# Kernel optimization log

Measured on AMD Instinct MI355X. Metric: run time of the kernel, lower is better.

The kernel has to match this reference:

```python
import jax, jax.numpy as jnp
import numpy as np

B, L, D_MODEL = 8, 2048, 512
N_QUBITS, Q_LAYERS = 10, 4
DIM = 2 ** N_QUBITS
EPS = 1e-5  # torch LayerNorm default


def _apply_1q_tok(state, U, q):
    # per-token 2x2 gate U: (N,2,2), wire 0 = most significant (PennyLane order)
    N = state.shape[0]
    s = state.reshape(N, 2 ** q, 2, -1)
    return jnp.einsum('nij,najb->naib', U, s).reshape(N, -1)


def _apply_1q(state, U, q):
    # shared 2x2 gate U: (2,2)
    N = state.shape[0]
    s = state.reshape(N, 2 ** q, 2, -1)
    return jnp.einsum('ij,najb->naib', U, s).reshape(N, -1)


def _cnot(state, c, t):
    N = state.shape[0]
    lo, hi = min(c, t), max(c, t)
    s = state.reshape(N, 2 ** lo, 2, 2 ** (hi - lo - 1), 2, -1)
    if c < t:
        # control is the first 2-axis; flip target axis where control==1
        s = s.at[:, :, 1].set(jnp.flip(s[:, :, 1], axis=3))
    else:
        # target is the first 2-axis, control the second
        s = s.at[:, :, :, :, 1].set(jnp.flip(s[:, :, :, :, 1], axis=2))
    return s.reshape(N, -1)


def _simulate(feats, weights):
    # feats: (N, n_qubits) angles; weights: (q_layers, n_qubits, 2)
    N = feats.shape[0]
    half = 0.5 * feats
    cxa = jnp.cos(half).astype(jnp.complex64)
    sxa = jnp.sin(half).astype(jnp.complex64)
    phz = jnp.exp(1j * half.astype(jnp.complex64))  # e^{+i theta/2}
    state = jnp.zeros((N, DIM), jnp.complex64).at[:, 0].set(1.0 + 0j)
    for l in range(Q_LAYERS):
        # AngleEmbedding rotation='X' : RX(feat_q) on wire q
        for q in range(N_QUBITS):
            c, s = cxa[:, q], sxa[:, q]
            U = jnp.stack([jnp.stack([c, -1j * s], -1),
                           jnp.stack([-1j * s, c], -1)], -2)  # (N,2,2)
            state = _apply_1q_tok(state, U, q)
        # AngleEmbedding rotation='Z' : RZ(feat_q) on wire q (diagonal)
        for q in range(N_QUBITS):
            p = phz[:, q]
            diag = jnp.stack([jnp.conj(p), p], -1)  # (N,2)
            s = state.reshape(N, 2 ** q, 2, -1)
            state = (s * diag[:, None, :, None]).reshape(N, -1)
        # trainable RY, RZ per wire (shared across tokens)
        for q in range(N_QUBITS):
            ty = 0.5 * weights[l, q, 0]
            cy, sy = jnp.cos(ty), jnp.sin(ty)
            Uy = jnp.stack([jnp.stack([cy, -sy]), jnp.stack([sy, cy])]).astype(jnp.complex64)
            state = _apply_1q(state, Uy, q)
            pz = jnp.exp(1j * (0.5 * weights[l, q, 1]).astype(jnp.complex64))
            diag = jnp.stack([jnp.conj(pz), pz])  # (2,)
            s = state.reshape(N, 2 ** q, 2, -1)
            state = (s * diag[None, None, :, None]).reshape(N, -1)
        # entangling CNOT ring
        for q in range(N_QUBITS):
            state = _cnot(state, q, (q + 1) % N_QUBITS)
    probs = jnp.real(state) ** 2 + jnp.imag(state) ** 2  # (N, 2**n)
    zs = []
    for q in range(N_QUBITS):
        p = probs.reshape(N, 2 ** q, 2, -1).sum(axis=(1, 3))  # (N,2)
        zs.append(p[:, 0] - p[:, 1])  # <Z_q>
    return jnp.stack(zs, -1)  # (N, n_qubits)


def setup_inputs() -> dict:
    key = jax.random.key(0)
    ks = jax.random.split(key, 4)
    x = jax.random.normal(ks[0], (B, L, D_MODEL), jnp.float32)
    in_W = jax.random.normal(ks[1], (N_QUBITS, D_MODEL), jnp.float32) / np.float32(np.sqrt(D_MODEL))
    in_b = jnp.zeros((N_QUBITS,), jnp.float32)
    gamma = jnp.ones((N_QUBITS,), jnp.float32)
    beta = jnp.zeros((N_QUBITS,), jnp.float32)
    weights = 0.05 * jax.random.normal(ks[2], (Q_LAYERS, N_QUBITS, 2), jnp.float32)
    out_W = jax.random.normal(ks[3], (D_MODEL, N_QUBITS), jnp.float32) / np.float32(np.sqrt(N_QUBITS))
    out_b = jnp.zeros((D_MODEL,), jnp.float32)
    return {"x": x, "in_W": in_W, "in_b": in_b, "gamma": gamma, "beta": beta,
            "weights": weights, "out_W": out_W, "out_b": out_b}


def reference(x, in_W, in_b, gamma, beta, weights, out_W, out_b):
    Bs, Ls, _ = x.shape
    h = jnp.tanh(jnp.einsum('bld,qd->blq', x, in_W) + in_b)
    mu = h.mean(-1, keepdims=True)
    var = ((h - mu) ** 2).mean(-1, keepdims=True)
    h = (h - mu) / jnp.sqrt(var + EPS) * gamma + beta
    q_out = _simulate(h.reshape(Bs * Ls, N_QUBITS), weights)
    q_out = q_out.reshape(Bs, Ls, N_QUBITS).astype(x.dtype)
    return x + jnp.einsum('blq,dq->bld', q_out, out_W) + out_b
```

## Files before the change

kernel.cpp:

```cpp
#include <hip/hip_runtime.h>

#define NQ 10
#define DQ 512
#define QL 4
#define NTOK (8 * 2048)
#define QOFF (NQ * DQ)
#define QHOFF (QOFF + 480)

typedef float v2f __attribute__((ext_vector_type(2)));
typedef float v4f __attribute__((ext_vector_type(4)));
typedef _Float16 h2 __attribute__((ext_vector_type(2)));

__device__ __forceinline__ int bperm(int addr, int v) {
    return __builtin_amdgcn_ds_bpermute(addr, v);
}
__device__ __forceinline__ float bpermf(int addr, float v) {
    return __builtin_bit_cast(float, bperm(addr, __builtin_bit_cast(int, v)));
}
__device__ __forceinline__ h2 bpermh(int addr, h2 v) {
    return __builtin_bit_cast(h2, bperm(addr, __builtin_bit_cast(int, v)));
}
template <int CTRL>
__device__ __forceinline__ int dppi(int i) {
    return __builtin_amdgcn_update_dpp(i, i, CTRL, 0xF, 0xF, false);
}
template <int M>
__device__ __forceinline__ float dppxf(float v) {
    int i = __builtin_bit_cast(int, v);
    if constexpr (M == 1)      i = dppi<0xB1>(i);
    else if constexpr (M == 2) i = dppi<0x4E>(i);
    else                       i = dppi<0x128>(i);
    return __builtin_bit_cast(float, i);
}
template <int M>
__device__ __forceinline__ h2 dppxh(h2 v) {
    int i = __builtin_bit_cast(int, v);
    if constexpr (M == 1)      i = dppi<0xB1>(i);
    else if constexpr (M == 2) i = dppi<0x4E>(i);
    else                       i = dppi<0x128>(i);
    return __builtin_bit_cast(h2, i);
}

__device__ __forceinline__ void reduce10(float* z, int a32, int a16, int a4) {
#pragma unroll
    for (int q = 0; q < NQ; ++q) {
        z[q] += bpermf(a32, z[q]);
        z[q] += bpermf(a16, z[q]);
        z[q] += dppxf<8>(z[q]);
        z[q] += bpermf(a4, z[q]);
        z[q] += dppxf<2>(z[q]);
        z[q] += dppxf<1>(z[q]);
    }
}

__device__ __forceinline__ h2 pk2(float a, float b) {
    return __builtin_bit_cast(h2, __builtin_amdgcn_cvt_pkrtz(a, b));
}
__device__ __forceinline__ h2 h2swap(h2 v) {
    return __builtin_shufflevector(v, v, 1, 0);
}
__device__ __forceinline__ h2 splat_lo(h2 v) {
    return __builtin_shufflevector(v, v, 0, 0);
}
__device__ __forceinline__ h2 splat_hi(h2 v) {
    return __builtin_shufflevector(v, v, 1, 1);
}

__device__ __forceinline__ v4f coef(const v4f* Q, float A, float C) {
    return Q[0] + A * Q[1] + C * Q[2];
}
__device__ __forceinline__ void coefh(const h2* Qg6, h2 A2, h2 C2,
                                      h2& arai, h2& brbi) {
    arai = Qg6[0] + A2 * Qg6[2] + C2 * Qg6[4];
    brbi = Qg6[1] + A2 * Qg6[3] + C2 * Qg6[5];
}

__device__ __forceinline__ void gate_lane_hp(h2* sr, h2* si, h2 arai, h2 brbi,
                                             bool bit, int addr) {
    const h2 ar = splat_lo(arai), ai = splat_hi(arai);
    const h2 br = splat_lo(brbi), bi = splat_hi(brbi);
    const h2 Ai = bit ? -ai : ai;
    const h2 Br = bit ? br : -br;
#pragma unroll
    for (int j = 0; j < 8; ++j) {
        h2 wr = bpermh(addr, sr[j]), wi = bpermh(addr, si[j]);
        h2 nr = ar * sr[j] - Ai * si[j] + Br * wr - bi * wi;
        h2 ni = ar * si[j] + Ai * sr[j] + Br * wi + bi * wr;
        sr[j] = nr; si[j] = ni;
    }
}
template <int M>
__device__ __forceinline__ void gate_lane_hd(h2* sr, h2* si, h2 arai, h2 brbi,
                                             bool bit) {
    const h2 ar = splat_lo(arai), ai = splat_hi(arai);
    const h2 br = splat_lo(brbi), bi = splat_hi(brbi);
    const h2 Ai = bit ? -ai : ai;
    const h2 Br = bit ? br : -br;
#pragma unroll
    for (int j = 0; j < 8; ++j) {
        h2 wr = dppxh<M>(sr[j]), wi = dppxh<M>(si[j]);
        h2 nr = ar * sr[j] - Ai * si[j] + Br * wr - bi * wi;
        h2 ni = ar * si[j] + Ai * sr[j] + Br * wi + bi * wr;
        sr[j] = nr; si[j] = ni;
    }
}
template <int BJ>
__device__ __forceinline__ void gate_reg_h(h2* sr, h2* si, h2 arai, h2 brbi) {
    const h2 ar = splat_lo(arai), ai = splat_hi(arai);
    const h2 br = splat_lo(brbi), bi = splat_hi(brbi);
#pragma unroll
    for (int j = 0; j < 8; ++j) if (!(j & BJ)) {
        const int j1 = j | BJ;
        h2 x0r = sr[j], x0i = si[j], x1r = sr[j1], x1i = si[j1];
        sr[j]  = ar * x0r - ai * x0i - br * x1r - bi * x1i;
        si[j]  = ar * x0i + ai * x0r - br * x1i + bi * x1r;
        sr[j1] = br * x0r - bi * x0i + ar * x1r + ai * x1i;
        si[j1] = br * x0i + bi * x0r + ar * x1i - ai * x1r;
    }
}
__device__ __forceinline__ void gate_elem_h(h2* sr, h2* si, h2 arai, h2 brbi) {
    const h2 ar = splat_lo(arai), bi = splat_hi(brbi);
    const h2 aiV = __builtin_bit_cast(h2,
        __builtin_bit_cast(int, splat_hi(arai)) ^ (int)0x80000000);
    const h2 brV = __builtin_bit_cast(h2,
        __builtin_bit_cast(int, splat_lo(brbi)) ^ 0x00008000);
#pragma unroll
    for (int j = 0; j < 8; ++j) {
        h2 swr = h2swap(sr[j]), swi = h2swap(si[j]);
        h2 nr = ar * sr[j] - aiV * si[j] + brV * swr - bi * swi;
        h2 ni = ar * si[j] + aiV * sr[j] + brV * swi + bi * swr;
        sr[j] = nr; si[j] = ni;
    }
}

__device__ __forceinline__ void perm678_h(h2* a) {
    h2 o2 = a[2], o4 = a[4], o7 = a[7];
    a[1] = h2swap(a[1]);
    a[2] = a[3]; a[3] = h2swap(o2);
    a[4] = a[6]; a[6] = a[5]; a[5] = h2swap(o7); a[7] = h2swap(o4);
}

__device__ __forceinline__ void cnot_ring_h(h2* sr, h2* si, int lane, int apm, int a32) {
#pragma unroll
    for (int j = 0; j < 8; ++j) {
        sr[j] = bpermh(apm, sr[j]);
        si[j] = bpermh(apm, si[j]);
    }
    {
        const bool ctrl = (lane & 1);
#pragma unroll
        for (int j = 0; j < 4; ++j) {
            h2 t0 = sr[j], t1 = sr[j + 4];
            sr[j] = ctrl ? t1 : t0; sr[j + 4] = ctrl ? t0 : t1;
            t0 = si[j]; t1 = si[j + 4];
            si[j] = ctrl ? t1 : t0; si[j + 4] = ctrl ? t0 : t1;
        }
    }
    perm678_h(sr);
    perm678_h(si);
#pragma unroll
    for (int j = 0; j < 8; ++j) {
        h2 w = bpermh(a32, sr[j]); sr[j] = (h2){sr[j].x, w.y};
        w = bpermh(a32, si[j]);    si[j] = (h2){si[j].x, w.y};
    }
}

__global__ __launch_bounds__(512) void prep_kernel(
    const float* __restrict__ weights, const float* __restrict__ out_W,
    float* __restrict__ ws)
{
    const int t = threadIdx.x;
#pragma unroll
    for (int q = 0; q < NQ; ++q)
        ws[q * DQ + t] = out_W[t * NQ + q];
    if (t < QL * NQ) {
        float w0 = weights[t * 2], w1 = weights[t * 2 + 1];
        float cy = __cosf(0.5f * w0), sy = __sinf(0.5f * w0);
        float cz = __cosf(0.5f * w1), sz = __sinf(0.5f * w1);
        float d = cy - sy, e = cy + sy;
        v4f q0 = (v4f){-cz * sy,  sz * sy,  cz * cy,  sz * cy};
        v4f q1 = (v4f){ cz * e,  -sz * e,  -cz * d,  -sz * d};
        v4f q2 = (v4f){-sz * d,  -cz * d,   sz * e,  -cz * e};
        v4f* Q = (v4f*)(ws + QOFF);
        Q[t * 3 + 0] = q0; Q[t * 3 + 1] = q1; Q[t * 3 + 2] = q2;
        h2* Qh = (h2*)(ws + QHOFF);
        Qh[t * 6 + 0] = pk2(q0.x, q0.y); Qh[t * 6 + 1] = pk2(q0.z, q0.w);
        Qh[t * 6 + 2] = pk2(q1.x, q1.y); Qh[t * 6 + 3] = pk2(q1.z, q1.w);
        Qh[t * 6 + 4] = pk2(q2.x, q2.y); Qh[t * 6 + 5] = pk2(q2.z, q2.w);
    }
}

__global__ __launch_bounds__(256) void quantum_kernel(
    const float* __restrict__ x, const float* __restrict__ in_W,
    const float* __restrict__ in_b, const float* __restrict__ gamma,
    const float* __restrict__ beta, const float* __restrict__ ws,
    const float* __restrict__ out_b, float* __restrict__ out)
{
    const int t = threadIdx.x;
    const int lane = t & 63;
    const int tok = blockIdx.x * 4 + (t >> 6);
    const v4f* Qg = (const v4f*)(ws + QOFF);
    const h2*  Qh = (const h2*)(ws + QHOFF);

    const int a32 = (lane ^ 32) << 2;
    const int a16 = (lane ^ 16) << 2;
    const int a4  = (lane ^ 4)  << 2;
    int srcl = lane;
#pragma unroll
    for (int q = 4; q >= 0; --q) {
        const int bc = 5 - q, bt = bc - 1;
        srcl ^= ((srcl >> bc) & 1) << bt;
    }
    const int apm = srcl << 2;

    const v4f* xrow4 = (const v4f*)(x + (size_t)tok * DQ);
    const v4f* inW4 = (const v4f*)in_W;
    v4f hv[NQ];
#pragma unroll
    for (int q = 0; q < NQ; ++q) hv[q] = (v4f){0.f, 0.f, 0.f, 0.f};
#pragma unroll
    for (int k = 0; k < 2; ++k) {
        v4f xk = xrow4[lane + 64 * k];
#pragma unroll
        for (int q = 0; q < NQ; ++q)
            hv[q] = xk * inW4[q * (DQ / 4) + lane + 64 * k] + hv[q];
    }
    float h[NQ];
#pragma unroll
    for (int q = 0; q < NQ; ++q)
        h[q] = (hv[q].x + hv[q].y) + (hv[q].z + hv[q].w);
    reduce10(h, a32, a16, a4);

    float mu = 0.f;
#pragma unroll
    for (int q = 0; q < NQ; ++q) {
        float e = __expf(2.f * (h[q] + in_b[q]));
        h[q] = (e - 1.f) * __builtin_amdgcn_rcpf(e + 1.f);
        mu += h[q];
    }
    mu *= 0.1f;
    float var = 0.f;
#pragma unroll
    for (int q = 0; q < NQ; ++q) { float d0 = h[q] - mu; var += d0 * d0; }
    var *= 0.1f;
    const float rstd = rsqrtf(var + 1e-5f);

    float Aq[NQ], Cq[NQ];
    h2 A2[NQ], C2[NQ];
#pragma unroll
    for (int q = 0; q < NQ; ++q) {
        float f = (h[q] - mu) * rstd * gamma[q] + beta[q];
        float hf = 0.5f * f;
        float c = __cosf(hf), s = __sinf(hf);
        Aq[q] = c * c;
        Cq[q] = c * s;
        A2[q] = pk2(Aq[q], Aq[q]);
        C2[q] = pk2(Cq[q], Cq[q]);
    }

    h2 sr[8], si[8];
    {
        const v4f* Q0 = Qg;
        v4f f0 = coef(Q0 + 0, Aq[0], Cq[0]);
        bool b0 = (lane & 32);
        float Lr = b0 ? f0.z : f0.x, Li = b0 ? f0.w : f0.y;
#pragma unroll
        for (int q = 1; q < 6; ++q) {
            v4f f = coef(Q0 + 3 * q, Aq[q], Cq[q]);
            bool b = lane & (1 << (5 - q));
            float fr = b ? f.z : f.x, fi = b ? f.w : f.y;
            float nr = Lr * fr - Li * fi, ni = Lr * fi + Li * fr;
            Lr = nr; Li = ni;
        }
        float Pr[8], Pi[8];
        {
            v4f f6 = coef(Q0 + 18, Aq[6], Cq[6]);
            Pr[0] = Lr * f6.x - Li * f6.y; Pi[0] = Lr * f6.y + Li * f6.x;
            Pr[4] = Lr * f6.z - Li * f6.w; Pi[4] = Lr * f6.w + Li * f6.z;
        }
        {
            v4f f7 = coef(Q0 + 21, Aq[7], Cq[7]);
#pragma unroll
            for (int jj = 0; jj < 8; jj += 4) {
                float tr1 = Pr[jj] * f7.z - Pi[jj] * f7.w;
                float ti1 = Pr[jj] * f7.w + Pi[jj] * f7.z;
                float tr0 = Pr[jj] * f7.x - Pi[jj] * f7.y;
                float ti0 = Pr[jj] * f7.y + Pi[jj] * f7.x;
                Pr[jj] = tr0; Pi[jj] = ti0; Pr[jj + 2] = tr1; Pi[jj + 2] = ti1;
            }
        }
        {
            v4f f8 = coef(Q0 + 24, Aq[8], Cq[8]);
#pragma unroll
            for (int jj = 0; jj < 8; jj += 2) {
                float tr1 = Pr[jj] * f8.z - Pi[jj] * f8.w;
                float ti1 = Pr[jj] * f8.w + Pi[jj] * f8.z;
                float tr0 = Pr[jj] * f8.x - Pi[jj] * f8.y;
                float ti0 = Pr[jj] * f8.y + Pi[jj] * f8.x;
                Pr[jj] = tr0; Pi[jj] = ti0; Pr[jj + 1] = tr1; Pi[jj + 1] = ti1;
            }
        }
        {
            v4f f9 = coef(Q0 + 27, Aq[9], Cq[9]);
#pragma unroll
            for (int j = 0; j < 8; ++j) {
                float e0r = Pr[j] * f9.x - Pi[j] * f9.y;
                float e0i = Pr[j] * f9.y + Pi[j] * f9.x;
                float e1r = Pr[j] * f9.z - Pi[j] * f9.w;
                float e1i = Pr[j] * f9.w + Pi[j] * f9.z;
                sr[j] = pk2(e0r, e1r);
                si[j] = pk2(e0i, e1i);
            }
        }
    }
    cnot_ring_h(sr, si, lane, apm, a32);

#pragma unroll
    for (int l = 1; l < QL; ++l) {
        const h2* Ql = Qh + l * NQ * 6;
        h2 arai, brbi;
        coefh(Ql + 0 * 6, A2[0], C2[0], arai, brbi); gate_lane_hp(sr, si, arai, brbi, lane & 32, a32);
        coefh(Ql + 2 * 6, A2[2], C2[2], arai, brbi); gate_lane_hd<8>(sr, si, arai, brbi, lane & 8);
        coefh(Ql + 1 * 6, A2[1], C2[1], arai, brbi); gate_lane_hp(sr, si, arai, brbi, lane & 16, a16);
        coefh(Ql + 4 * 6, A2[4], C2[4], arai, brbi); gate_lane_hd<2>(sr, si, arai, brbi, lane & 2);
        coefh(Ql + 3 * 6, A2[3], C2[3], arai, brbi); gate_lane_hp(sr, si, arai, brbi, lane & 4, a4);
        coefh(Ql + 5 * 6, A2[5], C2[5], arai, brbi); gate_lane_hd<1>(sr, si, arai, brbi, lane & 1);
        coefh(Ql + 6 * 6, A2[6], C2[6], arai, brbi); gate_reg_h<4>(sr, si, arai, brbi);
        coefh(Ql + 7 * 6, A2[7], C2[7], arai, brbi); gate_reg_h<2>(sr, si, arai, brbi);
        coefh(Ql + 8 * 6, A2[8], C2[8], arai, brbi); gate_reg_h<1>(sr, si, arai, brbi);
        coefh(Ql + 9 * 6, A2[9], C2[9], arai, brbi); gate_elem_h(sr, si, arai, brbi);
        if (l < QL - 1) cnot_ring_h(sr, si, lane, apm, a32);
    }

    h2 aP = (h2){0, 0}, a6 = (h2){0, 0}, a7 = (h2){0, 0}, aT = (h2){0, 0};
#pragma unroll
    for (int j = 0; j < 8; ++j) {
        h2 p = sr[j] * sr[j] + si[j] * si[j];
        aP += p;
        if (j & 4) a6 -= p; else a6 += p;
        if (((j >> 2) ^ (j >> 1)) & 1) a7 -= p; else a7 += p;
        if (((j >> 2) ^ (j >> 1) ^ j) & 1) aT -= p; else aT += p;
    }
    const float A0 = (float)aP.x + (float)aP.y;
    const float B6 = (float)a6.x + (float)a6.y;
    const float B7 = (float)a7.x + (float)a7.y;
    const float B8 = (float)aT.x + (float)aT.y;
    const float B9 = (float)aT.x - (float)aT.y;
    const bool P1 = __popc(lane & 0x30) & 1;
    const bool P2 = __popc(lane & 0x38) & 1;
    const bool P3 = __popc(lane & 0x3C) & 1;
    const bool P4 = __popc(lane & 0x3E) & 1;
    const bool P5 = __popc(lane & 0x3F) & 1;
    const bool PX = __popc(lane & 0x1F) & 1;
    float z[NQ];
    z[0] = PX ? -B9 : B9;
    z[1] = P1 ? -A0 : A0;
    z[2] = P2 ? -A0 : A0;
    z[3] = P3 ? -A0 : A0;
    z[4] = P4 ? -A0 : A0;
    z[5] = P5 ? -A0 : A0;
    z[6] = P5 ? -B6 : B6;
    z[7] = P5 ? -B7 : B7;
    z[8] = P5 ? -B8 : B8;
    z[9] = P5 ? -B9 : B9;

    h2 zp[5];
#pragma unroll
    for (int i = 0; i < 5; ++i) zp[i] = pk2(z[2 * i], z[2 * i + 1]);
#pragma unroll
    for (int i = 0; i < 5; ++i) {
        zp[i] += bpermh(a32, zp[i]);
        zp[i] += bpermh(a16, zp[i]);
        zp[i] += dppxh<8>(zp[i]);
        zp[i] += bpermh(a4, zp[i]);
        zp[i] += dppxh<2>(zp[i]);
        zp[i] += dppxh<1>(zp[i]);
    }
    float zf[NQ];
#pragma unroll
    for (int i = 0; i < 5; ++i) {
        zf[2 * i]     = (float)zp[i].x;
        zf[2 * i + 1] = (float)zp[i].y;
    }

    v4f* orow4 = (v4f*)(out + (size_t)tok * DQ);
    const v4f* ob4 = (const v4f*)out_b;
    const v4f* oWt4 = (const v4f*)ws;
#pragma unroll
    for (int k = 0; k < 2; ++k) {
        const int d4 = lane + 64 * k;
        v4f acc = xrow4[d4] + ob4[d4];
#pragma unroll
        for (int q = 0; q < NQ; ++q)
            acc = zf[q] * oWt4[q * (DQ / 4) + d4] + acc;
        orow4[d4] = acc;
    }
}

extern "C" void kernel_launch(void* const* d_in, const int* in_sizes, int n_in,
                              void* d_out, int out_size, void* d_ws, size_t ws_size,
                              hipStream_t stream) {
    const float* x       = (const float*)d_in[0];
    const float* in_W    = (const float*)d_in[1];
    const float* in_b    = (const float*)d_in[2];
    const float* gamma   = (const float*)d_in[3];
    const float* beta    = (const float*)d_in[4];
    const float* weights = (const float*)d_in[5];
    const float* out_W   = (const float*)d_in[6];
    const float* out_b   = (const float*)d_in[7];
    float* out = (float*)d_out;
    float* ws = (float*)d_ws;

    hipLaunchKernelGGL(prep_kernel, dim3(1), dim3(512), 0, stream,
                       weights, out_W, ws);
    hipLaunchKernelGGL(quantum_kernel, dim3(NTOK / 4), dim3(256), 0, stream,
                       x, in_W, in_b, gamma, beta, ws, out_b, out);
}
```

Before: 190.9 us.

## Process two tokens per wavefront to interleave independent state-vector work

Each wavefront now simulates two tokens at once, keeping two state vectors in registers and interleaving their gate, shuffle and reduction steps. The goal is more instruction-level parallelism to hide ds_bpermute/DPP latency, plus sharing in_W, out_W and per-layer gate coefficient loads between the two tokens. The grid is halved and the layer loop is no longer unrolled. This roughly doubles register pressure, which can lower occupancy or cause spills.

```diff
diff --git a/kernel.cpp b/kernel.cpp
--- a/kernel.cpp
+++ b/kernel.cpp
@@ -41,9 +41,10 @@
     return __builtin_bit_cast(h2, i);
 }
 
-__device__ __forceinline__ void reduce10(float* z, int a32, int a16, int a4) {
-#pragma unroll
-    for (int q = 0; q < NQ; ++q) {
+template <int N>
+__device__ __forceinline__ void reduceNf(float* z, int a32, int a16, int a4) {
+#pragma unroll
+    for (int q = 0; q < N; ++q) {
         z[q] += bpermf(a32, z[q]);
         z[q] += bpermf(a16, z[q]);
         z[q] += dppxf<8>(z[q]);
@@ -69,67 +70,100 @@
 __device__ __forceinline__ v4f coef(const v4f* Q, float A, float C) {
     return Q[0] + A * Q[1] + C * Q[2];
 }
-__device__ __forceinline__ void coefh(const h2* Qg6, h2 A2, h2 C2,
-                                      h2& arai, h2& brbi) {
-    arai = Qg6[0] + A2 * Qg6[2] + C2 * Qg6[4];
-    brbi = Qg6[1] + A2 * Qg6[3] + C2 * Qg6[5];
-}
-
-__device__ __forceinline__ void gate_lane_hp(h2* sr, h2* si, h2 arai, h2 brbi,
-                                             bool bit, int addr) {
-    const h2 ar = splat_lo(arai), ai = splat_hi(arai);
-    const h2 br = splat_lo(brbi), bi = splat_hi(brbi);
-    const h2 Ai = bit ? -ai : ai;
-    const h2 Br = bit ? br : -br;
-#pragma unroll
-    for (int j = 0; j < 8; ++j) {
-        h2 wr = bpermh(addr, sr[j]), wi = bpermh(addr, si[j]);
-        h2 nr = ar * sr[j] - Ai * si[j] + Br * wr - bi * wi;
-        h2 ni = ar * si[j] + Ai * sr[j] + Br * wi + bi * wr;
-        sr[j] = nr; si[j] = ni;
-    }
+__device__ __forceinline__ void coefh2(const h2* Qg6, const h2 AC[2][NQ], int q,
+                                       h2* arai, h2* brbi) {
+    const h2 q0 = Qg6[0], q1 = Qg6[1], q2 = Qg6[2];
+    const h2 q3 = Qg6[3], q4 = Qg6[4], q5 = Qg6[5];
+#pragma unroll
+    for (int tt = 0; tt < 2; ++tt) {
+        h2 A2 = splat_lo(AC[tt][q]), C2 = splat_hi(AC[tt][q]);
+        arai[tt] = q0 + A2 * q2 + C2 * q4;
+        brbi[tt] = q1 + A2 * q3 + C2 * q5;
+    }
+}
+
+__device__ __forceinline__ void gate_lane_hp2(h2 (&sr)[2][8], h2 (&si)[2][8],
+                                              const h2* arai, const h2* brbi,
+                                              bool bit, int addr) {
+    h2 ar[2], br[2], bi[2], Ai[2], Br[2];
+#pragma unroll
+    for (int tt = 0; tt < 2; ++tt) {
+        ar[tt] = splat_lo(arai[tt]);
+        h2 ai = splat_hi(arai[tt]);
+        br[tt] = splat_lo(brbi[tt]);
+        bi[tt] = splat_hi(brbi[tt]);
+        Ai[tt] = bit ? -ai : ai;
+        Br[tt] = bit ? br[tt] : -br[tt];
+    }
+#pragma unroll
+    for (int j = 0; j < 8; ++j)
+#pragma unroll
+        for (int tt = 0; tt < 2; ++tt) {
+            h2 wr = bpermh(addr, sr[tt][j]), wi = bpermh(addr, si[tt][j]);
+            h2 nr = ar[tt] * sr[tt][j] - Ai[tt] * si[tt][j] + Br[tt] * wr - bi[tt] * wi;
+            h2 ni = ar[tt] * si[tt][j] + Ai[tt] * sr[tt][j] + Br[tt] * wi + bi[tt] * wr;
+            sr[tt][j] = nr; si[tt][j] = ni;
+        }
 }
 template <int M>
-__device__ __forceinline__ void gate_lane_hd(h2* sr, h2* si, h2 arai, h2 brbi,
-                                             bool bit) {
-    const h2 ar = splat_lo(arai), ai = splat_hi(arai);
-    const h2 br = splat_lo(brbi), bi = splat_hi(brbi);
-    const h2 Ai = bit ? -ai : ai;
-    const h2 Br = bit ? br : -br;
-#pragma unroll
-    for (int j = 0; j < 8; ++j) {
-        h2 wr = dppxh<M>(sr[j]), wi = dppxh<M>(si[j]);
-        h2 nr = ar * sr[j] - Ai * si[j] + Br * wr - bi * wi;
-        h2 ni = ar * si[j] + Ai * sr[j] + Br * wi + bi * wr;
-        sr[j] = nr; si[j] = ni;
-    }
+__device__ __forceinline__ void gate_lane_hd2(h2 (&sr)[2][8], h2 (&si)[2][8],
+                                              const h2* arai, const h2* brbi,
+                                              bool bit) {
+    h2 ar[2], br[2], bi[2], Ai[2], Br[2];
+#pragma unroll
+    for (int tt = 0; tt < 2; ++tt) {
+        ar[tt] = splat_lo(arai[tt]);
+        h2 ai = splat_hi(arai[tt]);
+        br[tt] = splat_lo(brbi[tt]);
+        bi[tt] = splat_hi(brbi[tt]);
+        Ai[tt] = bit ? -ai : ai;
+        Br[tt] = bit ? br[tt] : -br[tt];
+    }
+#pragma unroll
+    for (int j = 0; j < 8; ++j)
+#pragma unroll
+        for (int tt = 0; tt < 2; ++tt) {
+            h2 wr = dppxh<M>(sr[tt][j]), wi = dppxh<M>(si[tt][j]);
+            h2 nr = ar[tt] * sr[tt][j] - Ai[tt] * si[tt][j] + Br[tt] * wr - bi[tt] * wi;
+            h2 ni = ar[tt] * si[tt][j] + Ai[tt] * sr[tt][j] + Br[tt] * wi + bi[tt] * wr;
+            sr[tt][j] = nr; si[tt][j] = ni;
+        }
 }
 template <int BJ>
-__device__ __forceinline__ void gate_reg_h(h2* sr, h2* si, h2 arai, h2 brbi) {
-    const h2 ar = splat_lo(arai), ai = splat_hi(arai);
-    const h2 br = splat_lo(brbi), bi = splat_hi(brbi);
-#pragma unroll
-    for (int j = 0; j < 8; ++j) if (!(j & BJ)) {
-        const int j1 = j | BJ;
-        h2 x0r = sr[j], x0i = si[j], x1r = sr[j1], x1i = si[j1];
-        sr[j]  = ar * x0r - ai * x0i - br * x1r - bi * x1i;
-        si[j]  = ar * x0i + ai * x0r - br * x1i + bi * x1r;
-        sr[j1] = br * x0r - bi * x0i + ar * x1r + ai * x1i;
-        si[j1] = br * x0i + bi * x0r + ar * x1i - ai * x1r;
-    }
-}
-__device__ __forceinline__ void gate_elem_h(h2* sr, h2* si, h2 arai, h2 brbi) {
-    const h2 ar = splat_lo(arai), bi = splat_hi(brbi);
-    const h2 aiV = __builtin_bit_cast(h2,
-        __builtin_bit_cast(int, splat_hi(arai)) ^ (int)0x80000000);
-    const h2 brV = __builtin_bit_cast(h2,
-        __builtin_bit_cast(int, splat_lo(brbi)) ^ 0x00008000);
-#pragma unroll
-    for (int j = 0; j < 8; ++j) {
-        h2 swr = h2swap(sr[j]), swi = h2swap(si[j]);
-        h2 nr = ar * sr[j] - aiV * si[j] + brV * swr - bi * swi;
-        h2 ni = ar * si[j] + aiV * sr[j] + brV * swi + bi * swr;
-        sr[j] = nr; si[j] = ni;
+__device__ __forceinline__ void gate_reg_h2(h2 (&sr)[2][8], h2 (&si)[2][8],
+                                            const h2* arai, const h2* brbi) {
+#pragma unroll
+    for (int tt = 0; tt < 2; ++tt) {
+        const h2 ar = splat_lo(arai[tt]), ai = splat_hi(arai[tt]);
+        const h2 br = splat_lo(brbi[tt]), bi = splat_hi(brbi[tt]);
+#pragma unroll
+        for (int j = 0; j < 8; ++j) if (!(j & BJ)) {
+            const int j1 = j | BJ;
+            h2 x0r = sr[tt][j], x0i = si[tt][j];
+            h2 x1r = sr[tt][j1], x1i = si[tt][j1];
+            sr[tt][j]  = ar * x0r - ai * x0i - br * x1r - bi * x1i;
+            si[tt][j]  = ar * x0i + ai * x0r - br * x1i + bi * x1r;
+            sr[tt][j1] = br * x0r - bi * x0i + ar * x1r + ai * x1i;
+            si[tt][j1] = br * x0i + bi * x0r + ar * x1i - ai * x1r;
+        }
+    }
+}
+__device__ __forceinline__ void gate_elem_h2(h2 (&sr)[2][8], h2 (&si)[2][8],
+                                             const h2* arai, const h2* brbi) {
+#pragma unroll
+    for (int tt = 0; tt < 2; ++tt) {
+        const h2 ar = splat_lo(arai[tt]), bi = splat_hi(brbi[tt]);
+        const h2 aiV = __builtin_bit_cast(h2,
+            __builtin_bit_cast(int, splat_hi(arai[tt])) ^ (int)0x80000000);
+        const h2 brV = __builtin_bit_cast(h2,
+            __builtin_bit_cast(int, splat_lo(brbi[tt])) ^ 0x00008000);
+#pragma unroll
+        for (int j = 0; j < 8; ++j) {
+            h2 swr = h2swap(sr[tt][j]), swi = h2swap(si[tt][j]);
+            h2 nr = ar * sr[tt][j] - aiV * si[tt][j] + brV * swr - bi * swi;
+            h2 ni = ar * si[tt][j] + aiV * sr[tt][j] + brV * swi + bi * swr;
+            sr[tt][j] = nr; si[tt][j] = ni;
+        }
     }
 }
 
@@ -140,28 +174,94 @@
     a[4] = a[6]; a[6] = a[5]; a[5] = h2swap(o7); a[7] = h2swap(o4);
 }
 
-__device__ __forceinline__ void cnot_ring_h(h2* sr, h2* si, int lane, int apm, int a32) {
-#pragma unroll
-    for (int j = 0; j < 8; ++j) {
-        sr[j] = bpermh(apm, sr[j]);
-        si[j] = bpermh(apm, si[j]);
-    }
+__device__ __forceinline__ void cnot_ring2(h2 (&sr)[2][8], h2 (&si)[2][8],
+                                           int lane, int apm, int a32) {
+#pragma unroll
+    for (int j = 0; j < 8; ++j)
+#pragma unroll
+        for (int tt = 0; tt < 2; ++tt) {
+            sr[tt][j] = bpermh(apm, sr[tt][j]);
+            si[tt][j] = bpermh(apm, si[tt][j]);
+        }
     {
         const bool ctrl = (lane & 1);
 #pragma unroll
-        for (int j = 0; j < 4; ++j) {
-            h2 t0 = sr[j], t1 = sr[j + 4];
-            sr[j] = ctrl ? t1 : t0; sr[j + 4] = ctrl ? t0 : t1;
-            t0 = si[j]; t1 = si[j + 4];
-            si[j] = ctrl ? t1 : t0; si[j + 4] = ctrl ? t0 : t1;
-        }
-    }
-    perm678_h(sr);
-    perm678_h(si);
-#pragma unroll
-    for (int j = 0; j < 8; ++j) {
-        h2 w = bpermh(a32, sr[j]); sr[j] = (h2){sr[j].x, w.y};
-        w = bpermh(a32, si[j]);    si[j] = (h2){si[j].x, w.y};
+        for (int tt = 0; tt < 2; ++tt)
+#pragma unroll
+            for (int j = 0; j < 4; ++j) {
+                h2 t0 = sr[tt][j], t1 = sr[tt][j + 4];
+                sr[tt][j] = ctrl ? t1 : t0; sr[tt][j + 4] = ctrl ? t0 : t1;
+                t0 = si[tt][j]; t1 = si[tt][j + 4];
+                si[tt][j] = ctrl ? t1 : t0; si[tt][j + 4] = ctrl ? t0 : t1;
+            }
+    }
+#pragma unroll
+    for (int tt = 0; tt < 2; ++tt) {
+        perm678_h(sr[tt]);
+        perm678_h(si[tt]);
+    }
+#pragma unroll
+    for (int j = 0; j < 8; ++j)
+#pragma unroll
+        for (int tt = 0; tt < 2; ++tt) {
+            h2 w = bpermh(a32, sr[tt][j]); sr[tt][j] = (h2){sr[tt][j].x, w.y};
+            w = bpermh(a32, si[tt][j]);    si[tt][j] = (h2){si[tt][j].x, w.y};
+        }
+}
+
+__device__ __forceinline__ void build_product(h2* sr, h2* si, const v4f* Q0,
+                                              const float* Aq, const float* Cq,
+                                              int lane) {
+    v4f f0 = coef(Q0 + 0, Aq[0], Cq[0]);
+    bool b0 = (lane & 32);
+    float Lr = b0 ? f0.z : f0.x, Li = b0 ? f0.w : f0.y;
+#pragma unroll
+    for (int q = 1; q < 6; ++q) {
+        v4f f = coef(Q0 + 3 * q, Aq[q], Cq[q]);
+        bool b = lane & (1 << (5 - q));
+        float fr = b ? f.z : f.x, fi = b ? f.w : f.y;
+        float nr = Lr * fr - Li * fi, ni = Lr * fi + Li * fr;
+        Lr = nr; Li = ni;
+    }
+    float Pr[8], Pi[8];
+    {
+        v4f f6 = coef(Q0 + 18, Aq[6], Cq[6]);
+        Pr[0] = Lr * f6.x - Li * f6.y; Pi[0] = Lr * f6.y + Li * f6.x;
+        Pr[4] = Lr * f6.z - Li * f6.w; Pi[4] = Lr * f6.w + Li * f6.z;
+    }
+    {
+        v4f f7 = coef(Q0 + 21, Aq[7], Cq[7]);
+#pragma unroll
+        for (int jj = 0; jj < 8; jj += 4) {
+            float tr1 = Pr[jj] * f7.z - Pi[jj] * f7.w;
+            float ti1 = Pr[jj] * f7.w + Pi[jj] * f7.z;
+            float tr0 = Pr[jj] * f7.x - Pi[jj] * f7.y;
+            float ti0 = Pr[jj] * f7.y + Pi[jj] * f7.x;
+            Pr[jj] = tr0; Pi[jj] = ti0; Pr[jj + 2] = tr1; Pi[jj + 2] = ti1;
+        }
+    }
+    {
+        v4f f8 = coef(Q0 + 24, Aq[8], Cq[8]);
+#pragma unroll
+        for (int jj = 0; jj < 8; jj += 2) {
+            float tr1 = Pr[jj] * f8.z - Pi[jj] * f8.w;
+            float ti1 = Pr[jj] * f8.w + Pi[jj] * f8.z;
+            float tr0 = Pr[jj] * f8.x - Pi[jj] * f8.y;
+            float ti0 = Pr[jj] * f8.y + Pi[jj] * f8.x;
+            Pr[jj] = tr0; Pi[jj] = ti0; Pr[jj + 1] = tr1; Pi[jj + 1] = ti1;
+        }
+    }
+    {
+        v4f f9 = coef(Q0 + 27, Aq[9], Cq[9]);
+#pragma unroll
+        for (int j = 0; j < 8; ++j) {
+            float e0r = Pr[j] * f9.x - Pi[j] * f9.y;
+            float e0i = Pr[j] * f9.y + Pi[j] * f9.x;
+            float e1r = Pr[j] * f9.z - Pi[j] * f9.w;
+            float e1i = Pr[j] * f9.w + Pi[j] * f9.z;
+            sr[j] = pk2(e0r, e1r);
+            si[j] = pk2(e0i, e1i);
+        }
     }
 }
 
@@ -198,7 +298,7 @@
 {
     const int t = threadIdx.x;
     const int lane = t & 63;
-    const int tok = blockIdx.x * 4 + (t >> 6);
+    const int tok0 = (blockIdx.x * 4 + (t >> 6)) * 2;
     const v4f* Qg = (const v4f*)(ws + QOFF);
     const h2*  Qh = (const h2*)(ws + QHOFF);
 
@@ -213,162 +313,112 @@
     }
     const int apm = srcl << 2;
 
-    const v4f* xrow4 = (const v4f*)(x + (size_t)tok * DQ);
+    const v4f* xr0 = (const v4f*)(x + (size_t)tok0 * DQ);
+    const v4f* xr1 = (const v4f*)(x + (size_t)(tok0 + 1) * DQ);
     const v4f* inW4 = (const v4f*)in_W;
-    v4f hv[NQ];
-#pragma unroll
-    for (int q = 0; q < NQ; ++q) hv[q] = (v4f){0.f, 0.f, 0.f, 0.f};
-#pragma unroll
-    for (int k = 0; k < 2; ++k) {
-        v4f xk = xrow4[lane + 64 * k];
-#pragma unroll
-        for (int q = 0; q < NQ; ++q)
-            hv[q] = xk * inW4[q * (DQ / 4) + lane + 64 * k] + hv[q];
-    }
-    float h[NQ];
-#pragma unroll
-    for (int q = 0; q < NQ; ++q)
-        h[q] = (hv[q].x + hv[q].y) + (hv[q].z + hv[q].w);
-    reduce10(h, a32, a16, a4);
-
-    float mu = 0.f;
+    const v4f xk00 = xr0[lane], xk01 = xr0[lane + 64];
+    const v4f xk10 = xr1[lane], xk11 = xr1[lane + 64];
+    float h[2][NQ];
 #pragma unroll
     for (int q = 0; q < NQ; ++q) {
-        float e = __expf(2.f * (h[q] + in_b[q]));
-        h[q] = (e - 1.f) * __builtin_amdgcn_rcpf(e + 1.f);
-        mu += h[q];
-    }
-    mu *= 0.1f;
-    float var = 0.f;
-#pragma unroll
-    for (int q = 0; q < NQ; ++q) { float d0 = h[q] - mu; var += d0 * d0; }
-    var *= 0.1f;
-    const float rstd = rsqrtf(var + 1e-5f);
-
-    float Aq[NQ], Cq[NQ];
-    h2 A2[NQ], C2[NQ];
-#pragma unroll
-    for (int q = 0; q < NQ; ++q) {
-        float f = (h[q] - mu) * rstd * gamma[q] + beta[q];
-        float hf = 0.5f * f;
-        float c = __cosf(hf), s = __sinf(hf);
-        Aq[q] = c * c;
-        Cq[q] = c * s;
-        A2[q] = pk2(Aq[q], Aq[q]);
-        C2[q] = pk2(Cq[q], Cq[q]);
-    }
-
-    h2 sr[8], si[8];
-    {
-        const v4f* Q0 = Qg;
-        v4f f0 = coef(Q0 + 0, Aq[0], Cq[0]);
-        bool b0 = (lane & 32);
-        float Lr = b0 ? f0.z : f0.x, Li = b0 ? f0.w : f0.y;
-#pragma unroll
-        for (int q = 1; q < 6; ++q) {
-            v4f f = coef(Q0 + 3 * q, Aq[q], Cq[q]);
-            bool b = lane & (1 << (5 - q));
-            float fr = b ? f.z : f.x, fi = b ? f.w : f.y;
-            float nr = Lr * fr - Li * fi, ni = Lr * fi + Li * fr;
-            Lr = nr; Li = ni;
-        }
-        float Pr[8], Pi[8];
-        {
-            v4f f6 = coef(Q0 + 18, Aq[6], Cq[6]);
-            Pr[0] = Lr * f6.x - Li * f6.y; Pi[0] = Lr * f6.y + Li * f6.x;
-            Pr[4] = Lr * f6.z - Li * f6.w; Pi[4] = Lr * f6.w + Li * f6.z;
-        }
-        {
-            v4f f7 = coef(Q0 + 21, Aq[7], Cq[7]);
-#pragma unroll
-            for (int jj = 0; jj < 8; jj += 4) {
-                float tr1 = Pr[jj] * f7.z - Pi[jj] * f7.w;
-                float ti1 = Pr[jj] * f7.w + Pi[jj] * f7.z;
-                float tr0 = Pr[jj] * f7.x - Pi[jj] * f7.y;
-                float ti0 = Pr[jj] * f7.y + Pi[jj] * f7.x;
-                Pr[jj] = tr0; Pi[jj] = ti0; Pr[jj + 2] = tr1; Pi[jj + 2] = ti1;
-            }
-        }
-        {
-            v4f f8 = coef(Q0 + 24, Aq[8], Cq[8]);
-#pragma unroll
-            for (int jj = 0; jj < 8; jj += 2) {
-                float tr1 = Pr[jj] * f8.z - Pi[jj] * f8.w;
-                float ti1 = Pr[jj] * f8.w + Pi[jj] * f8.z;
-                float tr0 = Pr[jj] * f8.x - Pi[jj] * f8.y;
-                float ti0 = Pr[jj] * f8.y + Pi[jj] * f8.x;
-                Pr[jj] = tr0; Pi[jj] = ti0; Pr[jj + 1] = tr1; Pi[jj + 1] = ti1;
-            }
-        }
-        {
-            v4f f9 = coef(Q0 + 27, Aq[9], Cq[9]);
-#pragma unroll
-            for (int j = 0; j < 8; ++j) {
-                float e0r = Pr[j] * f9.x - Pi[j] * f9.y;
-                float e0i = Pr[j] * f9.y + Pi[j] * f9.x;
-                float e1r = Pr[j] * f9.z - Pi[j] * f9.w;
-                float e1i = Pr[j] * f9.w + Pi[j] * f9.z;
-                sr[j] = pk2(e0r, e1r);
-                si[j] = pk2(e0i, e1i);
-            }
-        }
-    }
-    cnot_ring_h(sr, si, lane, apm, a32);
-
-#pragma unroll
+        v4f w0 = inW4[q * (DQ / 4) + lane];
+        v4f w1 = inW4[q * (DQ / 4) + lane + 64];
+        v4f a0 = xk00 * w0 + xk01 * w1;
+        v4f a1 = xk10 * w0 + xk11 * w1;
+        h[0][q] = (a0.x + a0.y) + (a0.z + a0.w);
+        h[1][q] = (a1.x + a1.y) + (a1.z + a1.w);
+    }
+    reduceNf<2 * NQ>(&h[0][0], a32, a16, a4);
+
+    h2 AC[2][NQ];
+    h2 sr[2][8], si[2][8];
+#pragma unroll
+    for (int tt = 0; tt < 2; ++tt) {
+        float mu = 0.f;
+#pragma unroll
+        for (int q = 0; q < NQ; ++q) {
+            float e = __expf(2.f * (h[tt][q] + in_b[q]));
+            h[tt][q] = (e - 1.f) * __builtin_amdgcn_rcpf(e + 1.f);
+            mu += h[tt][q];
+        }
+        mu *= 0.1f;
+        float var = 0.f;
+#pragma unroll
+        for (int q = 0; q < NQ; ++q) { float d0 = h[tt][q] - mu; var += d0 * d0; }
+        var *= 0.1f;
+        const float rstd = rsqrtf(var + 1e-5f);
+
+        float Aq[NQ], Cq[NQ];
+#pragma unroll
+        for (int q = 0; q < NQ; ++q) {
+            float f = (h[tt][q] - mu) * rstd * gamma[q] + beta[q];
+            float hf = 0.5f * f;
+            float c = __cosf(hf), s = __sinf(hf);
+            Aq[q] = c * c;
+            Cq[q] = c * s;
+            AC[tt][q] = pk2(Aq[q], Cq[q]);
+        }
+        build_product(sr[tt], si[tt], Qg, Aq, Cq, lane);
+    }
+    cnot_ring2(sr, si, lane, apm, a32);
+
+#pragma unroll 1
     for (int l = 1; l < QL; ++l) {
         const h2* Ql = Qh + l * NQ * 6;
-        h2 arai, brbi;
-        coefh(Ql + 0 * 6, A2[0], C2[0], arai, brbi); gate_lane_hp(sr, si, arai, brbi, lane & 32, a32);
-        coefh(Ql + 2 * 6, A2[2], C2[2], arai, brbi); gate_lane_hd<8>(sr, si, arai, brbi, lane & 8);
-        coefh(Ql + 1 * 6, A2[1], C2[1], arai, brbi); gate_lane_hp(sr, si, arai, brbi, lane & 16, a16);
-        coefh(Ql + 4 * 6, A2[4], C2[4], arai, brbi); gate_lane_hd<2>(sr, si, arai, brbi, lane & 2);
-        coefh(Ql + 3 * 6, A2[3], C2[3], arai, brbi); gate_lane_hp(sr, si, arai, brbi, lane & 4, a4);
-        coefh(Ql + 5 * 6, A2[5], C2[5], arai, brbi); gate_lane_hd<1>(sr, si, arai, brbi, lane & 1);
-        coefh(Ql + 6 * 6, A2[6], C2[6], arai, brbi); gate_reg_h<4>(sr, si, arai, brbi);
-        coefh(Ql + 7 * 6, A2[7], C2[7], arai, brbi); gate_reg_h<2>(sr, si, arai, brbi);
-        coefh(Ql + 8 * 6, A2[8], C2[8], arai, brbi); gate_reg_h<1>(sr, si, arai, brbi);
-        coefh(Ql + 9 * 6, A2[9], C2[9], arai, brbi); gate_elem_h(sr, si, arai, brbi);
-        if (l < QL - 1) cnot_ring_h(sr, si, lane, apm, a32);
-    }
-
-    h2 aP = (h2){0, 0}, a6 = (h2){0, 0}, a7 = (h2){0, 0}, aT = (h2){0, 0};
-#pragma unroll
-    for (int j = 0; j < 8; ++j) {
-        h2 p = sr[j] * sr[j] + si[j] * si[j];
-        aP += p;
-        if (j & 4) a6 -= p; else a6 += p;
-        if (((j >> 2) ^ (j >> 1)) & 1) a7 -= p; else a7 += p;
-        if (((j >> 2) ^ (j >> 1) ^ j) & 1) aT -= p; else aT += p;
-    }
-    const float A0 = (float)aP.x + (float)aP.y;
-    const float B6 = (float)a6.x + (float)a6.y;
-    const float B7 = (float)a7.x + (float)a7.y;
-    const float B8 = (float)aT.x + (float)aT.y;
-    const float B9 = (float)aT.x - (float)aT.y;
+        h2 arai[2], brbi[2];
+        coefh2(Ql + 0 * 6, AC, 0, arai, brbi); gate_lane_hp2(sr, si, arai, brbi, lane & 32, a32);
+        coefh2(Ql + 2 * 6, AC, 2, arai, brbi); gate_lane_hd2<8>(sr, si, arai, brbi, lane & 8);
+        coefh2(Ql + 1 * 6, AC, 1, arai, brbi); gate_lane_hp2(sr, si, arai, brbi, lane & 16, a16);
+        coefh2(Ql + 4 * 6, AC, 4, arai, brbi); gate_lane_hd2<2>(sr, si, arai, brbi, lane & 2);
+        coefh2(Ql + 3 * 6, AC, 3, arai, brbi); gate_lane_hp2(sr, si, arai, brbi, lane & 4, a4);
+        coefh2(Ql + 5 * 6, AC, 5, arai, brbi); gate_lane_hd2<1>(sr, si, arai, brbi, lane & 1);
+        coefh2(Ql + 6 * 6, AC, 6, arai, brbi); gate_reg_h2<4>(sr, si, arai, brbi);
+        coefh2(Ql + 7 * 6, AC, 7, arai, brbi); gate_reg_h2<2>(sr, si, arai, brbi);
+        coefh2(Ql + 8 * 6, AC, 8, arai, brbi); gate_reg_h2<1>(sr, si, arai, brbi);
+        coefh2(Ql + 9 * 6, AC, 9, arai, brbi); gate_elem_h2(sr, si, arai, brbi);
+        if (l < QL - 1) cnot_ring2(sr, si, lane, apm, a32);
+    }
+
     const bool P1 = __popc(lane & 0x30) & 1;
     const bool P2 = __popc(lane & 0x38) & 1;
     const bool P3 = __popc(lane & 0x3C) & 1;
     const bool P4 = __popc(lane & 0x3E) & 1;
     const bool P5 = __popc(lane & 0x3F) & 1;
     const bool PX = __popc(lane & 0x1F) & 1;
-    float z[NQ];
-    z[0] = PX ? -B9 : B9;
-    z[1] = P1 ? -A0 : A0;
-    z[2] = P2 ? -A0 : A0;
-    z[3] = P3 ? -A0 : A0;
-    z[4] = P4 ? -A0 : A0;
-    z[5] = P5 ? -A0 : A0;
-    z[6] = P5 ? -B6 : B6;
-    z[7] = P5 ? -B7 : B7;
-    z[8] = P5 ? -B8 : B8;
-    z[9] = P5 ? -B9 : B9;
-
-    h2 zp[5];
-#pragma unroll
-    for (int i = 0; i < 5; ++i) zp[i] = pk2(z[2 * i], z[2 * i + 1]);
-#pragma unroll
-    for (int i = 0; i < 5; ++i) {
+    h2 zp[10];
+#pragma unroll
+    for (int tt = 0; tt < 2; ++tt) {
+        h2 aP = (h2){0, 0}, a6 = (h2){0, 0}, a7 = (h2){0, 0}, aT = (h2){0, 0};
+#pragma unroll
+        for (int j = 0; j < 8; ++j) {
+            h2 p = sr[tt][j] * sr[tt][j] + si[tt][j] * si[tt][j];
+            aP += p;
+            if (j & 4) a6 -= p; else a6 += p;
+            if (((j >> 2) ^ (j >> 1)) & 1) a7 -= p; else a7 += p;
+            if (((j >> 2) ^ (j >> 1) ^ j) & 1) aT -= p; else aT += p;
+        }
+        const float A0 = (float)aP.x + (float)aP.y;
+        const float B6 = (float)a6.x + (float)a6.y;
+        const float B7 = (float)a7.x + (float)a7.y;
+        const float B8 = (float)aT.x + (float)aT.y;
+        const float B9 = (float)aT.x - (float)aT.y;
+        float z[NQ];
+        z[0] = PX ? -B9 : B9;
+        z[1] = P1 ? -A0 : A0;
+        z[2] = P2 ? -A0 : A0;
+        z[3] = P3 ? -A0 : A0;
+        z[4] = P4 ? -A0 : A0;
+        z[5] = P5 ? -A0 : A0;
+        z[6] = P5 ? -B6 : B6;
+        z[7] = P5 ? -B7 : B7;
+        z[8] = P5 ? -B8 : B8;
+        z[9] = P5 ? -B9 : B9;
+#pragma unroll
+        for (int i = 0; i < 5; ++i) zp[tt * 5 + i] = pk2(z[2 * i], z[2 * i + 1]);
+    }
+
+#pragma unroll
+    for (int i = 0; i < 10; ++i) {
         zp[i] += bpermh(a32, zp[i]);
         zp[i] += bpermh(a16, zp[i]);
         zp[i] += dppxh<8>(zp[i]);
@@ -376,24 +426,33 @@
         zp[i] += dppxh<2>(zp[i]);
         zp[i] += dppxh<1>(zp[i]);
     }
-    float zf[NQ];
-#pragma unroll
-    for (int i = 0; i < 5; ++i) {
-        zf[2 * i]     = (float)zp[i].x;
-        zf[2 * i + 1] = (float)zp[i].y;
-    }
-
-    v4f* orow4 = (v4f*)(out + (size_t)tok * DQ);
+    float zf[2][NQ];
+#pragma unroll
+    for (int tt = 0; tt < 2; ++tt)
+#pragma unroll
+        for (int i = 0; i < 5; ++i) {
+            zf[tt][2 * i]     = (float)zp[tt * 5 + i].x;
+            zf[tt][2 * i + 1] = (float)zp[tt * 5 + i].y;
+        }
+
+    v4f* or0 = (v4f*)(out + (size_t)tok0 * DQ);
+    v4f* or1 = (v4f*)(out + (size_t)(tok0 + 1) * DQ);
     const v4f* ob4 = (const v4f*)out_b;
     const v4f* oWt4 = (const v4f*)ws;
 #pragma unroll
     for (int k = 0; k < 2; ++k) {
         const int d4 = lane + 64 * k;
-        v4f acc = xrow4[d4] + ob4[d4];
-#pragma unroll
-        for (int q = 0; q < NQ; ++q)
-            acc = zf[q] * oWt4[q * (DQ / 4) + d4] + acc;
-        orow4[d4] = acc;
+        const v4f b = ob4[d4];
+        v4f acc0 = xr0[d4] + b;
+        v4f acc1 = xr1[d4] + b;
+#pragma unroll
+        for (int q = 0; q < NQ; ++q) {
+            v4f w = oWt4[q * (DQ / 4) + d4];
+            acc0 = zf[0][q] * w + acc0;
+            acc1 = zf[1][q] * w + acc1;
+        }
+        or0[d4] = acc0;
+        or1[d4] = acc1;
     }
 }
 
@@ -413,6 +472,6 @@
 
     hipLaunchKernelGGL(prep_kernel, dim3(1), dim3(512), 0, stream,
                        weights, out_W, ws);
-    hipLaunchKernelGGL(quantum_kernel, dim3(NTOK / 4), dim3(256), 0, stream,
+    hipLaunchKernelGGL(quantum_kernel, dim3(NTOK / 8), dim3(256), 0, stream,
                        x, in_W, in_b, gamma, beta, ws, out_b, out);
 }
```

New measurement: 193.3 us, median of 2. No clear change (+1.3%).
